# Performance work log

Hardware: AMD Instinct MI355X
Metric: run time of the kernel (lower is better)

## Reference

```python
import jax, jax.numpy as jnp
import numpy as np

N_NODES = 8192
N_EDGES = 65536
IN_DIM = 768
HIDDEN = 4096
N_CLASSES = 16


def setup_inputs() -> dict:
    key = jax.random.key(0)
    k1, k2, k3, k4 = jax.random.split(key, 4)
    x = jax.random.normal(k1, (N_NODES, IN_DIM), dtype=jnp.float32)
    edge_index = jax.random.randint(k2, (2, N_EDGES), 0, N_NODES, dtype=jnp.int64)
    # Glorot-ish init scale
    W1 = jax.random.normal(k3, (IN_DIM, HIDDEN), dtype=jnp.float32) * (1.0 / np.sqrt(IN_DIM))
    b1 = jnp.zeros((HIDDEN,), dtype=jnp.float32)
    W2 = jax.random.normal(k4, (HIDDEN, N_CLASSES), dtype=jnp.float32) * (1.0 / np.sqrt(HIDDEN))
    b2 = jnp.zeros((N_CLASSES,), dtype=jnp.float32)
    return {"x": x, "edge_index": edge_index, "W1": W1, "b1": b1, "W2": W2, "b2": b2}


def reference(x, edge_index, W1, b1, W2, b2):
    # GCNConv (PyG defaults): add self-loops, symmetric deg^-1/2 normalization,
    # transform-then-aggregate, plus bias. Then ReLU -> (dropout=identity at
    # inference) -> Linear -> log_softmax.
    N = x.shape[0]
    loops = jnp.arange(N, dtype=edge_index.dtype)
    src = jnp.concatenate([edge_index[0], loops])  # [E+N]
    dst = jnp.concatenate([edge_index[1], loops])  # [E+N]

    h = x @ W1  # [N, HIDDEN] dense GEMM

    deg = jax.ops.segment_sum(jnp.ones_like(dst, dtype=h.dtype), dst, num_segments=N)
    dinv = jnp.where(deg > 0, jax.lax.rsqrt(jnp.maximum(deg, 1e-12)), 0.0)
    norm = dinv[src] * dinv[dst]  # [E+N]

    agg = jax.ops.segment_sum(h[src] * norm[:, None], dst, num_segments=N)  # [N, HIDDEN]
    h = jax.nn.relu(agg + b1)

    logits = h @ W2 + b2  # [N, N_CLASSES]
    return jax.nn.log_softmax(logits, axis=1)
```

## Files before the change

### kernel.cpp

```cpp
#include <hip/hip_runtime.h>

#define N_NODES   8192
#define N_EDGES   65536
#define IN_DIM    768
#define HIDDEN    4096
#define N_CLASSES 16
#define SLOTS     64

typedef unsigned short ushort_t;
typedef __attribute__((ext_vector_type(8))) short bf16x8;
typedef __attribute__((ext_vector_type(4))) float f32x4;

__device__ __forceinline__ ushort_t f2bf(float f) {
    union { float f; unsigned i; } v; v.f = f;
    unsigned r = v.i + 0x7FFFu + ((v.i >> 16) & 1u);
    return (ushort_t)(r >> 16);
}
__device__ __forceinline__ float bf2f(ushort_t u) {
    union { unsigned i; float f; } v; v.i = ((unsigned)u) << 16; return v.f;
}

#define GLD_LDS16(gp, lp) \
    __builtin_amdgcn_global_load_lds((const __attribute__((address_space(1))) void*)(gp), \
                                     (__attribute__((address_space(3))) void*)(lp), 16, 0, 0)

__device__ __forceinline__ int esrc(const int* ei, int f32mode, int e) {
    return f32mode ? ei[e] : ei[2 * e];
}
__device__ __forceinline__ int edst(const int* ei, int f32mode, int e) {
    return f32mode ? ei[N_EDGES + e] : ei[2 * N_EDGES + 2 * e];
}

__global__ __launch_bounds__(256) void setup_all(const float* __restrict__ x,
                                                 ushort_t* __restrict__ xbf,
                                                 const float* __restrict__ W1,
                                                 ushort_t* __restrict__ W1T,
                                                 const float* __restrict__ W2,
                                                 ushort_t* __restrict__ W2T,
                                                 const int* __restrict__ ei,
                                                 int* __restrict__ cnt,
                                                 int* __restrict__ slots,
                                                 int* __restrict__ flag) {
    int b = blockIdx.x, t = threadIdx.x;
    if (b < 16) {
        __shared__ ushort_t ld[16 * 257];
        int k0 = b * 256;
        const float4* src = (const float4*)(W2 + (long)(k0 + t) * N_CLASSES);
        #pragma unroll
        for (int j = 0; j < 4; j++) {
            float4 v = src[j];
            ld[(j * 4 + 0) * 257 + t] = f2bf(v.x);
            ld[(j * 4 + 1) * 257 + t] = f2bf(v.y);
            ld[(j * 4 + 2) * 257 + t] = f2bf(v.z);
            ld[(j * 4 + 3) * 257 + t] = f2bf(v.w);
        }
        __syncthreads();
        #pragma unroll
        for (int c = 0; c < 16; c++)
            W2T[c * HIDDEN + k0 + t] = ld[c * 257 + t];
    } else if (b < 1552) {
        long i = (long)(b - 16) * 1024 + t;
        #pragma unroll
        for (int p = 0; p < 4; p++) {
            float4 v = ((const float4*)x)[i + p * 256];
            ushort4 r = { f2bf(v.x), f2bf(v.y), f2bf(v.z), f2bf(v.w) };
            ((ushort4*)xbf)[i + p * 256] = r;
        }
    } else if (b < 4624) {
        __shared__ ushort_t tile[32][33];
        int bb = b - 1552;
        int n0 = (bb & 127) * 32, k0 = (bb >> 7) * 32;
        int tx = t & 31, ty = t >> 5;
        #pragma unroll
        for (int j = 0; j < 4; j++) {
            int k = ty * 4 + j;
            tile[k][tx] = f2bf(W1[(k0 + k) * HIDDEN + n0 + tx]);
        }
        __syncthreads();
        #pragma unroll
        for (int j = 0; j < 4; j++) {
            int n = ty * 4 + j;
            W1T[(n0 + n) * IN_DIM + k0 + tx] = tile[tx][n];
        }
    } else {
        __shared__ int sv[256];
        int v = 0;
        for (int e = t; e < 4096; e += 256) v |= ei[2 * e + 1];
        sv[t] = v;
        __syncthreads();
        for (int off = 128; off > 0; off >>= 1) {
            if (t < off) sv[t] |= sv[t + off];
            __syncthreads();
        }
        int f = (sv[0] != 0) ? 1 : 0;
        if (b == 4624 && t == 0) *flag = f;
        int e = (b - 4624) * 256 + t;
        int s = esrc(ei, f, e), d = edst(ei, f, e);
        int p = atomicAdd(&cnt[d], 1);
        if (p < SLOTS) slots[d * SLOTS + p] = s;
    }
}

__global__ __launch_bounds__(192) void aggregate(const ushort_t* __restrict__ xbf,
                                                 const int* __restrict__ cnt,
                                                 const int* __restrict__ slots,
                                                 const int* __restrict__ ei,
                                                 const int* __restrict__ flag,
                                                 ushort_t* __restrict__ xagg) {
    int w = threadIdx.x >> 6, l = threadIdx.x & 63;
    int d = blockIdx.x;
    int fo = w * 256 + l * 4;
    int cd = cnt[d];
    float wd = rsqrtf((float)(cd + 1));
    ushort4 sv = *(const ushort4*)(xbf + (long)d * IN_DIM + fo);
    float a0 = wd * bf2f(sv.x), a1 = wd * bf2f(sv.y);
    float a2 = wd * bf2f(sv.z), a3 = wd * bf2f(sv.w);

    if (cd <= SLOTS) {
        const int* sl = slots + d * SLOTS;
        int j = 0;
        for (; j + 4 <= cd; j += 4) {
            int s0 = sl[j], s1 = sl[j + 1], s2 = sl[j + 2], s3 = sl[j + 3];
            float w0 = rsqrtf((float)(cnt[s0] + 1));
            float w1 = rsqrtf((float)(cnt[s1] + 1));
            float w2 = rsqrtf((float)(cnt[s2] + 1));
            float w3 = rsqrtf((float)(cnt[s3] + 1));
            ushort4 v0 = *(const ushort4*)(xbf + (long)s0 * IN_DIM + fo);
            ushort4 v1 = *(const ushort4*)(xbf + (long)s1 * IN_DIM + fo);
            ushort4 v2 = *(const ushort4*)(xbf + (long)s2 * IN_DIM + fo);
            ushort4 v3 = *(const ushort4*)(xbf + (long)s3 * IN_DIM + fo);
            a0 = fmaf(w0, bf2f(v0.x), a0); a1 = fmaf(w0, bf2f(v0.y), a1);
            a2 = fmaf(w0, bf2f(v0.z), a2); a3 = fmaf(w0, bf2f(v0.w), a3);
            a0 = fmaf(w1, bf2f(v1.x), a0); a1 = fmaf(w1, bf2f(v1.y), a1);
            a2 = fmaf(w1, bf2f(v1.z), a2); a3 = fmaf(w1, bf2f(v1.w), a3);
            a0 = fmaf(w2, bf2f(v2.x), a0); a1 = fmaf(w2, bf2f(v2.y), a1);
            a2 = fmaf(w2, bf2f(v2.z), a2); a3 = fmaf(w2, bf2f(v2.w), a3);
            a0 = fmaf(w3, bf2f(v3.x), a0); a1 = fmaf(w3, bf2f(v3.y), a1);
            a2 = fmaf(w3, bf2f(v3.z), a2); a3 = fmaf(w3, bf2f(v3.w), a3);
        }
        for (; j < cd; j++) {
            int s = sl[j];
            float ws = rsqrtf((float)(cnt[s] + 1));
            ushort4 v = *(const ushort4*)(xbf + (long)s * IN_DIM + fo);
            a0 = fmaf(ws, bf2f(v.x), a0); a1 = fmaf(ws, bf2f(v.y), a1);
            a2 = fmaf(ws, bf2f(v.z), a2); a3 = fmaf(ws, bf2f(v.w), a3);
        }
    } else {
        int f = *flag;
        for (int e = 0; e < N_EDGES; e++) {
            if (edst(ei, f, e) == d) {
                int s = esrc(ei, f, e);
                float ws = rsqrtf((float)(cnt[s] + 1));
                ushort4 v = *(const ushort4*)(xbf + (long)s * IN_DIM + fo);
                a0 = fmaf(ws, bf2f(v.x), a0); a1 = fmaf(ws, bf2f(v.y), a1);
                a2 = fmaf(ws, bf2f(v.z), a2); a3 = fmaf(ws, bf2f(v.w), a3);
            }
        }
    }
    ushort4 r = { f2bf(a0 * wd), f2bf(a1 * wd), f2bf(a2 * wd), f2bf(a3 * wd) };
    *(ushort4*)(xagg + (long)d * IN_DIM + fo) = r;
}

__global__ __launch_bounds__(256) void gemm1_fused(const ushort_t* __restrict__ A,
                                                   const ushort_t* __restrict__ Bt,
                                                   const float* __restrict__ b1,
                                                   const ushort_t* __restrict__ W2T,
                                                   float* __restrict__ part) {
    __shared__ char smem[40960];
    ushort_t* ldsA = (ushort_t*)smem;
    ushort_t* ldsB = (ushort_t*)(smem + 16384);
    int bx = blockIdx.x & 31;
    int by = blockIdx.x >> 5;
    int m0 = by * 128, n0 = bx * 128;
    int t = threadIdx.x;
    int w = t >> 6, l = t & 63;
    int wm = w & 1, wn = w >> 1;
    int q = l >> 4, lm = l & 15;

    f32x4 acc[4][4] = {};

    int offA[4], offB[4];
    #pragma unroll
    for (int mt = 0; mt < 4; mt++) {
        int m = wm * 64 + mt * 16 + lm;
        offA[mt] = m * 32 + (q ^ ((m >> 1) & 3)) * 8;
    }
    #pragma unroll
    for (int nt = 0; nt < 4; nt++) {
        int n = wn * 64 + nt * 16 + lm;
        offB[nt] = n * 32 + (q ^ ((n >> 1) & 3)) * 8;
    }

    const ushort_t* pA[2][2];
    const ushort_t* pB[2][2];
    #pragma unroll
    for (int i = 0; i < 2; i++) {
        int L = i * 256 + t;
        int row = L >> 2;
        int cg = (L & 3) ^ ((row >> 1) & 3);
        const ushort_t* a0 = A + (long)(m0 + row) * IN_DIM + cg * 8;
        const ushort_t* b0 = Bt + (long)(n0 + row) * IN_DIM + cg * 8;
        pA[0][i] = a0;      pA[1][i] = a0 + 32;
        pB[0][i] = b0;      pB[1][i] = b0 + 32;
    }

    for (int it = 0; it < IN_DIM / 64; it++) {
        __syncthreads();
        #pragma unroll
        for (int i = 0; i < 2; i++) {
            GLD_LDS16(pA[0][i], ldsA + (i * 256 + w * 64) * 8);
            GLD_LDS16(pB[0][i], ldsB + (i * 256 + w * 64) * 8);
            GLD_LDS16(pA[1][i], ldsA + 4096 + (i * 256 + w * 64) * 8);
            GLD_LDS16(pB[1][i], ldsB + 4096 + (i * 256 + w * 64) * 8);
        }
        #pragma unroll
        for (int i = 0; i < 2; i++) {
            pA[0][i] += 64; pA[1][i] += 64;
            pB[0][i] += 64; pB[1][i] += 64;
        }
        __syncthreads();

        #pragma unroll
        for (int j = 0; j < 2; j++) {
            bf16x8 af[4], bfr[4];
            #pragma unroll
            for (int mt = 0; mt < 4; mt++)
                af[mt] = *(const bf16x8*)(ldsA + j * 4096 + offA[mt]);
            #pragma unroll
            for (int nt = 0; nt < 4; nt++)
                bfr[nt] = *(const bf16x8*)(ldsB + j * 4096 + offB[nt]);
            #pragma unroll
            for (int mt = 0; mt < 4; mt++)
                #pragma unroll
                for (int nt = 0; nt < 4; nt++)
                    acc[mt][nt] = __builtin_amdgcn_mfma_f32_16x16x32_bf16(af[mt], bfr[nt], acc[mt][nt], 0, 0, 0);
        }
    }

    __syncthreads();
    const int RP = 80;
    ushort_t* myhl = (ushort_t*)smem + w * 64 * RP;

    float bias[4];
    #pragma unroll
    for (int nt = 0; nt < 4; nt++) bias[nt] = b1[n0 + wn * 64 + nt * 16 + lm];

    #pragma unroll
    for (int mt = 0; mt < 4; mt++) {
        #pragma unroll
        for (int nt = 0; nt < 4; nt++) {
            #pragma unroll
            for (int r = 0; r < 4; r++) {
                float v = acc[mt][nt][r] + bias[nt];
                v = v > 0.0f ? v : 0.0f;
                myhl[(mt * 16 + q * 4 + r) * RP + nt * 16 + lm] = f2bf(v);
            }
        }
    }

    f32x4 acc2[4] = {};
    #pragma unroll
    for (int kk = 0; kk < 2; kk++) {
        bf16x8 bf2 = *(const bf16x8*)(W2T + (long)lm * HIDDEN + n0 + wn * 64 + kk * 32 + q * 8);
        #pragma unroll
        for (int mt = 0; mt < 4; mt++) {
            bf16x8 a2 = *(const bf16x8*)(myhl + (mt * 16 + lm) * RP + kk * 32 + q * 8);
            acc2[mt] = __builtin_amdgcn_mfma_f32_16x16x32_bf16(a2, bf2, acc2[mt], 0, 0, 0);
        }
    }

    float* psum = (float*)smem;
    __syncthreads();
    if (wn == 1) {
        #pragma unroll
        for (int mt = 0; mt < 4; mt++)
            #pragma unroll
            for (int r = 0; r < 4; r++)
                psum[(wm * 64 + mt * 16 + q * 4 + r) * 17 + lm] = acc2[mt][r];
    }
    __syncthreads();
    if (wn == 0) {
        float* pslab = part + ((long)bx * N_NODES + m0 + wm * 64) * N_CLASSES;
        #pragma unroll
        for (int mt = 0; mt < 4; mt++)
            #pragma unroll
            for (int r = 0; r < 4; r++) {
                float v = acc2[mt][r] + psum[(wm * 64 + mt * 16 + q * 4 + r) * 17 + lm];
                pslab[(mt * 16 + q * 4 + r) * N_CLASSES + lm] = v;
            }
    }
}

__global__ __launch_bounds__(256) void reduce_softmax(const float* __restrict__ part,
                                                      const float* __restrict__ b2,
                                                      float* __restrict__ out) {
    int t = threadIdx.x;
    int row = blockIdx.x * 16 + (t >> 4);
    int cls = t & 15;
    float v = b2[cls];
    #pragma unroll
    for (int s = 0; s < 32; s++)
        v += part[((long)s * N_NODES + row) * N_CLASSES + cls];
    float mx = v;
    #pragma unroll
    for (int off = 1; off < 16; off <<= 1)
        mx = fmaxf(mx, __shfl_xor(mx, off, 64));
    float e = __expf(v - mx);
    float sm = e;
    #pragma unroll
    for (int off = 1; off < 16; off <<= 1)
        sm += __shfl_xor(sm, off, 64);
    out[(long)row * N_CLASSES + cls] = v - mx - __logf(sm);
}


extern "C" void kernel_launch(void* const* d_in, const int* in_sizes, int n_in,
                              void* d_out, int out_size, void* d_ws, size_t ws_size,
                              hipStream_t stream) {
    const float* x  = (const float*)d_in[0];
    const int*   ei = (const int*)d_in[1];
    const float* W1 = (const float*)d_in[2];
    const float* b1 = (const float*)d_in[3];
    const float* W2 = (const float*)d_in[4];
    const float* b2 = (const float*)d_in[5];
    float* out = (float*)d_out;
    char* ws = (char*)d_ws;

    float*    part  = (float*)(ws);
    ushort_t* xagg  = (ushort_t*)(ws + 16777216);
    ushort_t* xbf   = (ushort_t*)(ws + 29360128);
    ushort_t* W1T   = (ushort_t*)(ws + 41943040);
    ushort_t* W2T   = (ushort_t*)(ws + 48234496);
    int*      cnt   = (int*)(ws + 48365568);
    int*      slots = (int*)(ws + 48398336);
    int*      flag  = (int*)(ws + 50495488);

    hipMemsetAsync(cnt, 0, 32768, stream);
    setup_all<<<4880, 256, 0, stream>>>(x, xbf, W1, W1T, W2, W2T, ei, cnt, slots, flag);
    aggregate<<<N_NODES, 192, 0, stream>>>(xbf, cnt, slots, ei, flag, xagg);
    gemm1_fused<<<(N_NODES / 128) * (HIDDEN / 128), 256, 0, stream>>>(xagg, W1T, b1, W2T, part);
    reduce_softmax<<<N_NODES / 16, 256, 0, stream>>>(part, b2, out);
}
```

Baseline: 177.3 us.

## Move W1 transpose into aggregate launch and shrink GEMM epilogue LDS

The W1 fp32-to-bf16 transpose moves out of the first setup kernel and into the aggregation kernel's grid, so it can overlap with the gather work and the setup launch shrinks. Separately, the fused GEMM epilogue now stages the ReLU'd hidden tile in two halves of 32 rows per wave, which cuts shared memory from 40 KB to 32 KB. Launch bounds now request 5 blocks per CU to raise occupancy. Risks are register spills under the tighter launch bound, and aggregation blocks wasting 64 idle threads each.

```diff
diff --git a/kernel.cpp b/kernel.cpp
--- a/kernel.cpp
+++ b/kernel.cpp
@@ -31,16 +31,14 @@
     return f32mode ? ei[N_EDGES + e] : ei[2 * N_EDGES + 2 * e];
 }
 
-__global__ __launch_bounds__(256) void setup_all(const float* __restrict__ x,
-                                                 ushort_t* __restrict__ xbf,
-                                                 const float* __restrict__ W1,
-                                                 ushort_t* __restrict__ W1T,
-                                                 const float* __restrict__ W2,
-                                                 ushort_t* __restrict__ W2T,
-                                                 const int* __restrict__ ei,
-                                                 int* __restrict__ cnt,
-                                                 int* __restrict__ slots,
-                                                 int* __restrict__ flag) {
+__global__ __launch_bounds__(256) void phase1(const float* __restrict__ x,
+                                              ushort_t* __restrict__ xbf,
+                                              const float* __restrict__ W2,
+                                              ushort_t* __restrict__ W2T,
+                                              const int* __restrict__ ei,
+                                              int* __restrict__ cnt,
+                                              int* __restrict__ slots,
+                                              int* __restrict__ flag) {
     int b = blockIdx.x, t = threadIdx.x;
     if (b < 16) {
         __shared__ ushort_t ld[16 * 257];
@@ -66,22 +64,6 @@
             ushort4 r = { f2bf(v.x), f2bf(v.y), f2bf(v.z), f2bf(v.w) };
             ((ushort4*)xbf)[i + p * 256] = r;
         }
-    } else if (b < 4624) {
-        __shared__ ushort_t tile[32][33];
-        int bb = b - 1552;
-        int n0 = (bb & 127) * 32, k0 = (bb >> 7) * 32;
-        int tx = t & 31, ty = t >> 5;
-        #pragma unroll
-        for (int j = 0; j < 4; j++) {
-            int k = ty * 4 + j;
-            tile[k][tx] = f2bf(W1[(k0 + k) * HIDDEN + n0 + tx]);
-        }
-        __syncthreads();
-        #pragma unroll
-        for (int j = 0; j < 4; j++) {
-            int n = ty * 4 + j;
-            W1T[(n0 + n) * IN_DIM + k0 + tx] = tile[tx][n];
-        }
     } else {
         __shared__ int sv[256];
         int v = 0;
@@ -93,22 +75,43 @@
             __syncthreads();
         }
         int f = (sv[0] != 0) ? 1 : 0;
-        if (b == 4624 && t == 0) *flag = f;
-        int e = (b - 4624) * 256 + t;
+        if (b == 1552 && t == 0) *flag = f;
+        int e = (b - 1552) * 256 + t;
         int s = esrc(ei, f, e), d = edst(ei, f, e);
         int p = atomicAdd(&cnt[d], 1);
         if (p < SLOTS) slots[d * SLOTS + p] = s;
     }
 }
 
-__global__ __launch_bounds__(192) void aggregate(const ushort_t* __restrict__ xbf,
-                                                 const int* __restrict__ cnt,
-                                                 const int* __restrict__ slots,
-                                                 const int* __restrict__ ei,
-                                                 const int* __restrict__ flag,
-                                                 ushort_t* __restrict__ xagg) {
-    int w = threadIdx.x >> 6, l = threadIdx.x & 63;
-    int d = blockIdx.x;
+__global__ __launch_bounds__(256) void phase2(const float* __restrict__ W1,
+                                              ushort_t* __restrict__ W1T,
+                                              const ushort_t* __restrict__ xbf,
+                                              const int* __restrict__ cnt,
+                                              const int* __restrict__ slots,
+                                              const int* __restrict__ ei,
+                                              const int* __restrict__ flag,
+                                              ushort_t* __restrict__ xagg) {
+    int b = blockIdx.x, t = threadIdx.x;
+    if (b < 3072) {
+        __shared__ ushort_t tile[32][33];
+        int n0 = (b & 127) * 32, k0 = (b >> 7) * 32;
+        int tx = t & 31, ty = t >> 5;
+        #pragma unroll
+        for (int j = 0; j < 4; j++) {
+            int k = ty * 4 + j;
+            tile[k][tx] = f2bf(W1[(k0 + k) * HIDDEN + n0 + tx]);
+        }
+        __syncthreads();
+        #pragma unroll
+        for (int j = 0; j < 4; j++) {
+            int n = ty * 4 + j;
+            W1T[(n0 + n) * IN_DIM + k0 + tx] = tile[tx][n];
+        }
+        return;
+    }
+    if (t >= 192) return;
+    int w = t >> 6, l = t & 63;
+    int d = b - 3072;
     int fo = w * 256 + l * 4;
     int cd = cnt[d];
     float wd = rsqrtf((float)(cd + 1));
@@ -161,12 +164,12 @@
     *(ushort4*)(xagg + (long)d * IN_DIM + fo) = r;
 }
 
-__global__ __launch_bounds__(256) void gemm1_fused(const ushort_t* __restrict__ A,
-                                                   const ushort_t* __restrict__ Bt,
-                                                   const float* __restrict__ b1,
-                                                   const ushort_t* __restrict__ W2T,
-                                                   float* __restrict__ part) {
-    __shared__ char smem[40960];
+__global__ __launch_bounds__(256, 5) void gemm1_fused(const ushort_t* __restrict__ A,
+                                                      const ushort_t* __restrict__ Bt,
+                                                      const float* __restrict__ b1,
+                                                      const ushort_t* __restrict__ W2T,
+                                                      float* __restrict__ part) {
+    __shared__ char smem[32768];
     ushort_t* ldsA = (ushort_t*)smem;
     ushort_t* ldsB = (ushort_t*)(smem + 16384);
     int bx = blockIdx.x & 31;
@@ -239,34 +242,40 @@
 
     __syncthreads();
     const int RP = 80;
-    ushort_t* myhl = (ushort_t*)smem + w * 64 * RP;
+    ushort_t* myhl = (ushort_t*)smem + w * 32 * RP;
 
     float bias[4];
     #pragma unroll
     for (int nt = 0; nt < 4; nt++) bias[nt] = b1[n0 + wn * 64 + nt * 16 + lm];
 
-    #pragma unroll
-    for (int mt = 0; mt < 4; mt++) {
-        #pragma unroll
-        for (int nt = 0; nt < 4; nt++) {
-            #pragma unroll
-            for (int r = 0; r < 4; r++) {
-                float v = acc[mt][nt][r] + bias[nt];
-                v = v > 0.0f ? v : 0.0f;
-                myhl[(mt * 16 + q * 4 + r) * RP + nt * 16 + lm] = f2bf(v);
+    bf16x8 bf2[2];
+    #pragma unroll
+    for (int kk = 0; kk < 2; kk++)
+        bf2[kk] = *(const bf16x8*)(W2T + (long)lm * HIDDEN + n0 + wn * 64 + kk * 32 + q * 8);
+
+    f32x4 acc2[4] = {};
+    #pragma unroll
+    for (int h = 0; h < 2; h++) {
+        #pragma unroll
+        for (int mt2 = 0; mt2 < 2; mt2++) {
+            int mt = h * 2 + mt2;
+            #pragma unroll
+            for (int nt = 0; nt < 4; nt++) {
+                #pragma unroll
+                for (int r = 0; r < 4; r++) {
+                    float v = acc[mt][nt][r] + bias[nt];
+                    v = v > 0.0f ? v : 0.0f;
+                    myhl[(mt2 * 16 + q * 4 + r) * RP + nt * 16 + lm] = f2bf(v);
+                }
             }
         }
-    }
-
-    f32x4 acc2[4] = {};
-    #pragma unroll
-    for (int kk = 0; kk < 2; kk++) {
-        bf16x8 bf2 = *(const bf16x8*)(W2T + (long)lm * HIDDEN + n0 + wn * 64 + kk * 32 + q * 8);
-        #pragma unroll
-        for (int mt = 0; mt < 4; mt++) {
-            bf16x8 a2 = *(const bf16x8*)(myhl + (mt * 16 + lm) * RP + kk * 32 + q * 8);
-            acc2[mt] = __builtin_amdgcn_mfma_f32_16x16x32_bf16(a2, bf2, acc2[mt], 0, 0, 0);
-        }
+        #pragma unroll
+        for (int kk = 0; kk < 2; kk++)
+            #pragma unroll
+            for (int mt2 = 0; mt2 < 2; mt2++) {
+                bf16x8 a2 = *(const bf16x8*)(myhl + (mt2 * 16 + lm) * RP + kk * 32 + q * 8);
+                acc2[h * 2 + mt2] = __builtin_amdgcn_mfma_f32_16x16x32_bf16(a2, bf2[kk], acc2[h * 2 + mt2], 0, 0, 0);
+            }
     }
 
     float* psum = (float*)smem;
@@ -336,8 +345,8 @@
     int*      flag  = (int*)(ws + 50495488);
 
     hipMemsetAsync(cnt, 0, 32768, stream);
-    setup_all<<<4880, 256, 0, stream>>>(x, xbf, W1, W1T, W2, W2T, ei, cnt, slots, flag);
-    aggregate<<<N_NODES, 192, 0, stream>>>(xbf, cnt, slots, ei, flag, xagg);
+    phase1<<<1808, 256, 0, stream>>>(x, xbf, W2, W2T, ei, cnt, slots, flag);
+    phase2<<<11264, 256, 0, stream>>>(W1, W1T, xbf, cnt, slots, ei, flag, xagg);
     gemm1_fused<<<(N_NODES / 128) * (HIDDEN / 128), 256, 0, stream>>>(xagg, W1T, b1, W2T, part);
     reduce_softmax<<<N_NODES / 16, 256, 0, stream>>>(part, b2, out);
 }
```

Result: slower. 283.0 us (+59.7%).
